# Kernel optimization log

Hardware: AMD Instinct MI355X
Metric: run time of the kernel (lower is better)

## Reference

```python
import jax, jax.numpy as jnp
import numpy as np

DIM = 1024
H = 16
HD = DIM // H          # head_dim = 64
SCALE = HD ** -0.5
LAMBDA_INIT = 0.1


def setup_inputs() -> dict:
    key = jax.random.key(0)
    ks = jax.random.split(key, 8)
    B, NQ, NKV = 4, 1024, 1024
    # xavier_uniform for linear weights; stored as (in, out) for x @ W
    def xavier(k, fan_in, fan_out):
        a = float(np.sqrt(6.0 / (fan_in + fan_out)))
        return jax.random.uniform(k, (fan_in, fan_out), jnp.float32, -a, a)
    return {
        "DriftData": jax.random.normal(ks[0], (B, NQ, DIM), jnp.float32),
        "OceanData": jax.random.normal(ks[1], (B, NKV, DIM), jnp.float32),
        "Wq": xavier(ks[2], DIM, 2 * DIM),
        "Wk": xavier(ks[3], DIM, 2 * DIM),
        "Wv": xavier(ks[4], DIM, DIM),
        "Wo": xavier(ks[5], DIM, DIM),
        "lambda_q1": jax.random.normal(ks[6], (H, HD), jnp.float32),
        "lambda_k1": jax.random.normal(jax.random.fold_in(ks[6], 1), (H, HD), jnp.float32),
        "lambda_q2": jax.random.normal(ks[7], (H, HD), jnp.float32),
        "lambda_k2": jax.random.normal(jax.random.fold_in(ks[7], 1), (H, HD), jnp.float32),
    }


def reference(DriftData, OceanData, Wq, Wk, Wv, Wo,
              lambda_q1, lambda_k1, lambda_q2, lambda_k2):
    B, NQ, dim = DriftData.shape
    NKV = OceanData.shape[1]
    # lambda scalar per head: exp(q1.k1) - exp(q2.k2) + lambda_init  -> (H,)
    lam = (jnp.exp(jnp.sum(lambda_q1 * lambda_k1, axis=-1))
           - jnp.exp(jnp.sum(lambda_q2 * lambda_k2, axis=-1)) + LAMBDA_INIT)
    # projections: Q,K -> 2*dim, V -> dim
    Q = (DriftData @ Wq).reshape(B, NQ, H, 2 * HD).transpose(0, 2, 1, 3)   # b h q 2hd
    K = (OceanData @ Wk).reshape(B, NKV, H, 2 * HD).transpose(0, 2, 1, 3)  # b h k 2hd
    V = (OceanData @ Wv).reshape(B, NKV, H, HD).transpose(0, 2, 1, 3)      # b h k hd
    Q1, Q2 = Q[..., :HD], Q[..., HD:]
    K1, K2 = K[..., :HD], K[..., HD:]
    A1 = jnp.einsum('bhqd,bhkd->bhqk', Q1, K1) * SCALE
    A2 = jnp.einsum('bhqd,bhkd->bhqk', Q2, K2) * SCALE
    att = jax.nn.softmax(A1, axis=-1) - lam[None, :, None, None] * jax.nn.softmax(A2, axis=-1)
    out = jnp.einsum('bhqk,bhkd->bhqd', att, V)            # b h q hd
    out = out.transpose(0, 2, 1, 3).reshape(B, NQ, dim)    # b q dim
    return out @ Wo
```

## Files before the change

kernel.cpp:

```cpp
#include <hip/hip_runtime.h>
#include <hip/hip_bf16.h>

typedef unsigned short u16;
typedef unsigned int u32;
typedef __attribute__((ext_vector_type(8))) short short8;
typedef __attribute__((ext_vector_type(4))) float f32x4;
typedef __attribute__((ext_vector_type(4))) u16 us4;

#define MFMA16(a,b,c) __builtin_amdgcn_mfma_f32_16x16x32_bf16(a,b,c,0,0,0)

__device__ __forceinline__ u16 f2b(float x){
  u32 u = __builtin_bit_cast(u32, x);
  u32 r = (u + 0x7fffu + ((u >> 16) & 1u)) >> 16;
  return (u16)r;
}
__device__ __forceinline__ u16 f2b_hw(float x){
  return __builtin_bit_cast(u16, __float2bfloat16(x));
}

__device__ __forceinline__ void gll16(const u16* g, u16* l){
  __builtin_amdgcn_global_load_lds((const __attribute__((address_space(1))) u32*)g,
                                   (__attribute__((address_space(3))) u32*)l, 16, 0, 0);
}

__global__ __launch_bounds__(256) void k_conv2(const float* __restrict__ a, const float* __restrict__ bsrc,
                                               u16* __restrict__ ya, u16* __restrict__ yb){
  int bid = blockIdx.x;
  const float* x = (bid < 4096) ? a : bsrc;
  u16* y = (bid < 4096) ? ya : yb;
  int i = (bid & 4095) * 256 + threadIdx.x;
  float4 v = reinterpret_cast<const float4*>(x)[i];
  us4 o; o.x = f2b(v.x); o.y = f2b(v.y); o.z = f2b(v.z); o.w = f2b(v.w);
  reinterpret_cast<us4*>(y)[i] = o;
}

__global__ __launch_bounds__(256) void k_prep_w(const float* __restrict__ Wq, const float* __restrict__ Wk,
                                                const float* __restrict__ Wv, const float* __restrict__ Wo,
                                                u16* __restrict__ WqT, u16* __restrict__ WkvT,
                                                u16* __restrict__ WoT,
                                                const float* __restrict__ lq1, const float* __restrict__ lk1,
                                                const float* __restrict__ lq2, const float* __restrict__ lk2,
                                                float* __restrict__ lam){
  __shared__ float t[32][33];
  const int z = blockIdx.z;
  const float* W; u16* WT; int N; float scale = 1.0f;
  if (z == 0){ W = Wq; WT = WqT; N = 2048; scale = 0.125f; }
  else if (z == 1){ W = Wk; WT = WkvT; N = 2048; }
  else if (z == 2){ W = Wv; WT = WkvT + 2048*1024; N = 1024; }
  else { W = Wo; WT = WoT; N = 1024; }
  int n0 = blockIdx.x * 32, k0 = blockIdx.y * 32;
  int tx = threadIdx.x & 31, ty = threadIdx.x >> 5;
  if (n0 < N){
    #pragma unroll
    for (int i = 0; i < 4; i++)
      t[ty + i*8][tx] = W[(size_t)(k0 + ty + i*8) * N + n0 + tx];
    __syncthreads();
    #pragma unroll
    for (int i = 0; i < 4; i++)
      WT[(size_t)(n0 + ty + i*8) * 1024 + k0 + tx] = f2b(t[tx][ty + i*8] * scale);
  }
  if (z == 3 && blockIdx.x == 0 && blockIdx.y == 0 && threadIdx.x < 16){
    int h = threadIdx.x;
    float d1 = 0.f, d2 = 0.f;
    for (int i = 0; i < 64; i++){
      d1 += lq1[h*64 + i] * lk1[h*64 + i];
      d2 += lq2[h*64 + i] * lk2[h*64 + i];
    }
    lam[h] = expf(d1) - expf(d2) + 0.1f;
  }
}

__global__ __launch_bounds__(256) void k_transpose_v(const u16* __restrict__ KV, u16* __restrict__ VT){
  __shared__ u16 t[32][34];
  int kv0 = blockIdx.x * 32, d0 = blockIdx.y * 32, bh = blockIdx.z;
  int b = bh >> 4, h = bh & 15;
  int tx = threadIdx.x & 31, ty = threadIdx.x >> 5;
  #pragma unroll
  for (int i = 0; i < 4; i++)
    t[ty + i*8][tx] = KV[(size_t)(b*1024 + kv0 + ty + i*8) * 3072 + 2048 + h*64 + d0 + tx];
  __syncthreads();
  #pragma unroll
  for (int i = 0; i < 4; i++)
    VT[(size_t)bh * 65536 + (size_t)(d0 + ty + i*8) * 1024 + kv0 + tx] = t[tx][ty + i*8];
}

template<bool OUTF32>
__device__ __forceinline__ void gemm_body(const u16* __restrict__ A, const u16* __restrict__ B,
                                          void* __restrict__ C, int N, int m0, int n0,
                                          u16* As, u16* Bs){
  const int tid = threadIdx.x;
  const int wave = tid >> 6, lane = tid & 63;
  const int lr = lane & 15, lg = lane >> 4;
  const int wm = wave >> 1, wn = wave & 1;

  f32x4 acc[4][4];
  #pragma unroll
  for (int i = 0; i < 4; i++)
    #pragma unroll
    for (int j = 0; j < 4; j++){ f32x4 z = {0.f,0.f,0.f,0.f}; acc[i][j] = z; }

  const int srow = tid >> 3;
  const int skc  = tid & 7;

  for (int k0 = 0; k0 < 1024; k0 += 64){
    #pragma unroll
    for (int c = 0; c < 4; c++){
      int row = c*32 + srow;
      const u16* ga = A + (size_t)(m0 + row) * 1024 + k0 + ((skc ^ (row & 7)) << 3);
      gll16(ga, As + c*2048 + wave*512);
      const u16* gb = B + (size_t)(n0 + row) * 1024 + k0 + ((skc ^ (row & 7)) << 3);
      gll16(gb, Bs + c*2048 + wave*512);
    }
    __syncthreads();
    #pragma unroll
    for (int kc = 0; kc < 2; kc++){
      short8 af[4], bfr[4];
      #pragma unroll
      for (int mt = 0; mt < 4; mt++){
        int row = wm*64 + mt*16 + lr;
        af[mt] = *reinterpret_cast<const short8*>(As + row*64 + (((kc*4 + lg) ^ (row & 7)) << 3));
      }
      #pragma unroll
      for (int nt = 0; nt < 4; nt++){
        int rown = wn*64 + nt*16 + lr;
        bfr[nt] = *reinterpret_cast<const short8*>(Bs + rown*64 + (((kc*4 + lg) ^ (rown & 7)) << 3));
      }
      #pragma unroll
      for (int mt = 0; mt < 4; mt++)
        #pragma unroll
        for (int nt = 0; nt < 4; nt++)
          acc[mt][nt] = MFMA16(af[mt], bfr[nt], acc[mt][nt]);
    }
    __syncthreads();
  }
  #pragma unroll
  for (int mt = 0; mt < 4; mt++)
    #pragma unroll
    for (int nt = 0; nt < 4; nt++)
      #pragma unroll
      for (int r = 0; r < 4; r++){
        int row = m0 + wm*64 + mt*16 + lg*4 + r;
        int col = n0 + wn*64 + nt*16 + lr;
        if (OUTF32) ((float*)C)[(size_t)row * N + col] = acc[mt][nt][r];
        else        ((u16*)C)[(size_t)row * N + col] = f2b(acc[mt][nt][r]);
      }
}

__global__ __launch_bounds__(256) void k_gemm_proj(const u16* __restrict__ Xd, const u16* __restrict__ Xo,
                                                   const u16* __restrict__ WqT, const u16* __restrict__ WkvT,
                                                   u16* __restrict__ Qb, u16* __restrict__ KVb){
  __shared__ __align__(16) u16 As[128*64];
  __shared__ __align__(16) u16 Bs[128*64];
  int bid = blockIdx.x;
  if (bid < 512){
    gemm_body<false>(Xd, WqT, Qb, 2048, (bid >> 4) * 128, (bid & 15) * 128, As, Bs);
  } else {
    int t = bid - 512;
    gemm_body<false>(Xo, WkvT, KVb, 3072, (t / 24) * 128, (t % 24) * 128, As, Bs);
  }
}

__global__ __launch_bounds__(256) void k_gemm_out(const u16* __restrict__ A, const u16* __restrict__ B,
                                                  float* __restrict__ C){
  __shared__ __align__(16) u16 As[128*64];
  __shared__ __align__(16) u16 Bs[128*64];
  int bid = blockIdx.x;
  gemm_body<true>(A, B, C, 1024, (bid >> 3) * 128, (bid & 7) * 128, As, Bs);
}

__device__ __forceinline__ void softmax_t(f32x4 s[4], float& m, float& l, f32x4 (&ob)[4][2], int qt,
                                          u16* pl, int lr, int lg){
  float a0 = fmaxf(fmaxf(s[0][0], s[0][1]), fmaxf(s[0][2], s[0][3]));
  float a1 = fmaxf(fmaxf(s[1][0], s[1][1]), fmaxf(s[1][2], s[1][3]));
  float a2 = fmaxf(fmaxf(s[2][0], s[2][1]), fmaxf(s[2][2], s[2][3]));
  float a3 = fmaxf(fmaxf(s[3][0], s[3][1]), fmaxf(s[3][2], s[3][3]));
  float mx = fmaxf(fmaxf(a0, a1), fmaxf(a2, a3));
  mx = fmaxf(mx, __shfl_xor(mx, 16));
  mx = fmaxf(mx, __shfl_xor(mx, 32));
  if (__any(mx > m + 8.0f)){
    float nm = fmaxf(m, mx);
    float al = __expf(m - nm);
    m = nm; l *= al;
    #pragma unroll
    for (int nt = 0; nt < 4; nt++)
      #pragma unroll
      for (int r = 0; r < 4; r++) ob[nt][qt][r] *= al;
  }
  float sum = 0.f;
  #pragma unroll
  for (int nt = 0; nt < 4; nt++)
    #pragma unroll
    for (int r = 0; r < 4; r++){
      float p = __expf(s[nt][r] - m);
      s[nt][r] = p;
      sum += p;
    }
  sum += __shfl_xor(sum, 16);
  sum += __shfl_xor(sum, 32);
  l += sum;
  char* base = (char*)pl + lr * 128;
  const int swz = (lr & 7) << 4;
  #pragma unroll
  for (int nt = 0; nt < 4; nt++){
    us4 h;
    h.x = f2b_hw(s[nt][0]); h.y = f2b_hw(s[nt][1]);
    h.z = f2b_hw(s[nt][2]); h.w = f2b_hw(s[nt][3]);
    *reinterpret_cast<us4*>(base + ((nt*32 + lg*8) ^ swz)) = h;
  }
}

__global__ __launch_bounds__(256, 2) void k_attn(const u16* __restrict__ Q, const u16* __restrict__ KVb,
                                                 const u16* __restrict__ VT, const float* __restrict__ lam,
                                                 u16* __restrict__ O){
  int bid = blockIdx.x;
  int logical = (bid & 7) * 64 + (bid >> 3);
  int qt8 = logical & 7, h = (logical >> 3) & 15, b = logical >> 7;
  const int tid = threadIdx.x, wave = tid >> 6, lane = tid & 63;
  const int lr = lane & 15, lg = lane >> 4;
  const int qb = qt8 * 128 + wave * 32;

  __shared__ __align__(16) u16 Ks[2][8192];
  __shared__ __align__(16) u16 Vs[2][4096];
  __shared__ __align__(16) u16 Pl[4][2][2][1024];

  const int srow = tid >> 4, schunk = tid & 15;
  const int vrow = tid >> 3, vchunk = tid & 7;
  const u16* Kg = KVb + (size_t)(b*1024 + srow) * 3072 + h*128 + ((schunk ^ (srow & 7)) << 3);
  const u16* Vg = VT + (size_t)(b*16 + h) * 65536 + (size_t)vrow * 1024 + ((vchunk ^ (vrow & 7)) << 3);

  short8 qf[2][2][2];
  #pragma unroll
  for (int qt = 0; qt < 2; qt++){
    const u16* Qp = Q + (size_t)(b*1024 + qb + qt*16 + lr) * 2048 + h*128 + lg*8;
    #pragma unroll
    for (int kc = 0; kc < 2; kc++){
      qf[0][qt][kc] = *reinterpret_cast<const short8*>(Qp + kc*32);
      qf[1][qt][kc] = *reinterpret_cast<const short8*>(Qp + 64 + kc*32);
    }
  }
  const float lamh = lam[h];

  f32x4 o[2][4][2];
  #pragma unroll
  for (int br = 0; br < 2; br++)
    #pragma unroll
    for (int nt = 0; nt < 4; nt++)
      #pragma unroll
      for (int qt = 0; qt < 2; qt++){ f32x4 z = {0.f,0.f,0.f,0.f}; o[br][nt][qt] = z; }
  float m[2][2], l[2][2];
  #pragma unroll
  for (int br = 0; br < 2; br++)
    #pragma unroll
    for (int qt = 0; qt < 2; qt++){ m[br][qt] = -3.0e38f; l[br][qt] = 0.f; }

  auto STAGE = [&](int buf, int kv0){
    u16* kd = &Ks[buf][tid * 8];
    #pragma unroll
    for (int i = 0; i < 4; i++)
      gll16(Kg + (size_t)(kv0 + i*16) * 3072, kd + i*2048);
    u16* vd = &Vs[buf][tid * 8];
    #pragma unroll
    for (int j = 0; j < 2; j++)
      gll16(Vg + kv0 + (size_t)(j*32) * 1024, vd + j*2048);
  };

  STAGE(0, 0);
  __syncthreads();

  for (int t = 0; t < 16; t++){
    const int cur = t & 1;
    if (t < 15) STAGE(cur ^ 1, (t + 1) << 6);

    const u16* kbuf = &Ks[cur][0];
    const u16* vbuf = &Vs[cur][0];

    #pragma unroll
    for (int br = 0; br < 2; br++){
      short8 kf[4][2];
      #pragma unroll
      for (int nt = 0; nt < 4; nt++)
        #pragma unroll
        for (int kc = 0; kc < 2; kc++)
          kf[nt][kc] = *reinterpret_cast<const short8*>(
              kbuf + (nt*16 + lr)*128 + (((br*8 + kc*4 + lg) ^ (lr & 7)) << 3));
      #pragma unroll
      for (int qt = 0; qt < 2; qt++){
        f32x4 s[4];
        #pragma unroll
        for (int nt = 0; nt < 4; nt++){ f32x4 z = {0.f,0.f,0.f,0.f}; s[nt] = z; }
        #pragma unroll
        for (int nt = 0; nt < 4; nt++)
          #pragma unroll
          for (int kc = 0; kc < 2; kc++)
            s[nt] = MFMA16(kf[nt][kc], qf[br][qt][kc], s[nt]);
        softmax_t(s, m[br][qt], l[br][qt], o[br], qt, &Pl[wave][qt][br][0], lr, lg);
      }
    }

    const int swz = (lr & 7) << 4;
    #pragma unroll
    for (int kc = 0; kc < 2; kc++){
      short8 pf[2][2];
      #pragma unroll
      for (int qt = 0; qt < 2; qt++)
        #pragma unroll
        for (int br = 0; br < 2; br++)
          pf[qt][br] = *reinterpret_cast<const short8*>(
              (char*)&Pl[wave][qt][br][0] + lr*128 + ((kc*64 + lg*16) ^ swz));
      #pragma unroll
      for (int nt = 0; nt < 4; nt++){
        short8 vf = *reinterpret_cast<const short8*>(
            vbuf + (nt*16 + lr)*64 + (((kc*4 + lg) ^ (lr & 7)) << 3));
        #pragma unroll
        for (int qt = 0; qt < 2; qt++){
          o[0][nt][qt] = MFMA16(vf, pf[qt][0], o[0][nt][qt]);
          o[1][nt][qt] = MFMA16(vf, pf[qt][1], o[1][nt][qt]);
        }
      }
    }
    __syncthreads();
  }

  #pragma unroll
  for (int qt = 0; qt < 2; qt++){
    const float inv1 = 1.0f / l[0][qt];
    const float inv2 = lamh / l[1][qt];
    u16* Op = O + (size_t)(b*1024 + qb + qt*16 + lr) * 1024 + h*64;
    #pragma unroll
    for (int nt = 0; nt < 4; nt++){
      us4 hh;
      #pragma unroll
      for (int r = 0; r < 4; r++){
        float v = o[0][nt][qt][r] * inv1 - o[1][nt][qt][r] * inv2;
        ((u16*)&hh)[r] = f2b_hw(v);
      }
      *reinterpret_cast<us4*>(Op + nt*16 + lg*4) = hh;
    }
  }
}

extern "C" void kernel_launch(void* const* d_in, const int* in_sizes, int n_in,
                              void* d_out, int out_size, void* d_ws, size_t ws_size,
                              hipStream_t stream){
  const float* Drift = (const float*)d_in[0];
  const float* Ocean = (const float*)d_in[1];
  const float* Wq    = (const float*)d_in[2];
  const float* Wk    = (const float*)d_in[3];
  const float* Wv    = (const float*)d_in[4];
  const float* Wo    = (const float*)d_in[5];
  const float* lq1   = (const float*)d_in[6];
  const float* lk1   = (const float*)d_in[7];
  const float* lq2   = (const float*)d_in[8];
  const float* lk2   = (const float*)d_in[9];
  float* out = (float*)d_out;

  char* ws = (char*)d_ws;
  u16* Xd   = (u16*)(ws);
  u16* Xo   = (u16*)(ws + 8388608);
  u16* WqT  = (u16*)(ws + 16777216);
  u16* WkvT = (u16*)(ws + 20971520);
  u16* WoT  = (u16*)(ws + 27262976);
  u16* Qb   = (u16*)(ws + 29360128);
  u16* KVb  = (u16*)(ws + 46137344);
  u16* VTb  = (u16*)(ws + 71303168);
  u16* Ob   = (u16*)(ws + 79691776);
  float* lam = (float*)(ws + 88080384);

  k_conv2<<<8192, 256, 0, stream>>>(Drift, Ocean, Xd, Xo);
  k_prep_w<<<dim3(64,32,4), 256, 0, stream>>>(Wq, Wk, Wv, Wo, WqT, WkvT, WoT,
                                              lq1, lk1, lq2, lk2, lam);
  k_gemm_proj<<<1280, 256, 0, stream>>>(Xd, Xo, WqT, WkvT, Qb, KVb);
  k_transpose_v<<<dim3(32,2,64), 256, 0, stream>>>(KVb, VTb);
  k_attn<<<512, 256, 0, stream>>>(Qb, KVb, VTb, lam, Ob);
  k_gemm_out<<<256, 256, 0, stream>>>(Ob, WoT, out);
}
```

Before: 155.3 us.

## Fuse V transpose into projection GEMM epilogue, use exp2 softmax and MFMA priority

The V-column tiles of the KV projection GEMM now write their output directly in transposed head-major layout through an LDS staging epilogue. This removes the separate transpose kernel and its extra global round trip. The Q scale now folds in log2(e), so the softmax uses the hardware exp2 directly, and the rescale threshold is adjusted to match. s_setprio raises wave priority around the MFMA sections of attention. The costs are a more complex epilogue with extra barriers, and the KVb V-region is no longer written (attention reads VT only).

Result: slower. 163.0 us (+4.9%).

```diff
diff --git a/kernel.cpp b/kernel.cpp
--- a/kernel.cpp
+++ b/kernel.cpp
@@ -6,6 +6,7 @@
 typedef __attribute__((ext_vector_type(8))) short short8;
 typedef __attribute__((ext_vector_type(4))) float f32x4;
 typedef __attribute__((ext_vector_type(4))) u16 us4;
+typedef __attribute__((ext_vector_type(4))) u32 u32x4;
 
 #define MFMA16(a,b,c) __builtin_amdgcn_mfma_f32_16x16x32_bf16(a,b,c,0,0,0)
 
@@ -17,6 +18,7 @@
 __device__ __forceinline__ u16 f2b_hw(float x){
   return __builtin_bit_cast(u16, __float2bfloat16(x));
 }
+__device__ __forceinline__ float ex2(float x){ return __builtin_amdgcn_exp2f(x); }
 
 __device__ __forceinline__ void gll16(const u16* g, u16* l){
   __builtin_amdgcn_global_load_lds((const __attribute__((address_space(1))) u32*)g,
@@ -44,7 +46,7 @@
   __shared__ float t[32][33];
   const int z = blockIdx.z;
   const float* W; u16* WT; int N; float scale = 1.0f;
-  if (z == 0){ W = Wq; WT = WqT; N = 2048; scale = 0.125f; }
+  if (z == 0){ W = Wq; WT = WqT; N = 2048; scale = 0.1803368867f; }
   else if (z == 1){ W = Wk; WT = WkvT; N = 2048; }
   else if (z == 2){ W = Wv; WT = WkvT + 2048*1024; N = 1024; }
   else { W = Wo; WT = WoT; N = 1024; }
@@ -70,19 +72,45 @@
   }
 }
 
-__global__ __launch_bounds__(256) void k_transpose_v(const u16* __restrict__ KV, u16* __restrict__ VT){
-  __shared__ u16 t[32][34];
-  int kv0 = blockIdx.x * 32, d0 = blockIdx.y * 32, bh = blockIdx.z;
-  int b = bh >> 4, h = bh & 15;
-  int tx = threadIdx.x & 31, ty = threadIdx.x >> 5;
-  #pragma unroll
-  for (int i = 0; i < 4; i++)
-    t[ty + i*8][tx] = KV[(size_t)(b*1024 + kv0 + ty + i*8) * 3072 + 2048 + h*64 + d0 + tx];
-  __syncthreads();
-  #pragma unroll
-  for (int i = 0; i < 4; i++)
-    VT[(size_t)bh * 65536 + (size_t)(d0 + ty + i*8) * 1024 + kv0 + tx] = t[tx][ty + i*8];
-}
+#define GEMM_MAIN_LOOP(A_, B_, m0_, n0_)                                                \
+  f32x4 acc[4][4];                                                                      \
+  _Pragma("unroll")                                                                     \
+  for (int i = 0; i < 4; i++)                                                           \
+    _Pragma("unroll")                                                                   \
+    for (int j = 0; j < 4; j++){ f32x4 z = {0.f,0.f,0.f,0.f}; acc[i][j] = z; }          \
+  const int srow = tid >> 3;                                                            \
+  const int skc  = tid & 7;                                                             \
+  for (int k0 = 0; k0 < 1024; k0 += 64){                                                \
+    _Pragma("unroll")                                                                   \
+    for (int c = 0; c < 4; c++){                                                        \
+      int row = c*32 + srow;                                                            \
+      const u16* ga = (A_) + (size_t)((m0_) + row) * 1024 + k0 + ((skc ^ (row & 7)) << 3); \
+      gll16(ga, As + c*2048 + wave*512);                                                \
+      const u16* gb = (B_) + (size_t)((n0_) + row) * 1024 + k0 + ((skc ^ (row & 7)) << 3); \
+      gll16(gb, Bs + c*2048 + wave*512);                                                \
+    }                                                                                   \
+    __syncthreads();                                                                    \
+    _Pragma("unroll")                                                                   \
+    for (int kc = 0; kc < 2; kc++){                                                     \
+      short8 af[4], bfr[4];                                                             \
+      _Pragma("unroll")                                                                 \
+      for (int mt = 0; mt < 4; mt++){                                                   \
+        int row = wm*64 + mt*16 + lr;                                                   \
+        af[mt] = *reinterpret_cast<const short8*>(As + row*64 + (((kc*4 + lg) ^ (row & 7)) << 3)); \
+      }                                                                                 \
+      _Pragma("unroll")                                                                 \
+      for (int nt = 0; nt < 4; nt++){                                                   \
+        int rown = wn*64 + nt*16 + lr;                                                  \
+        bfr[nt] = *reinterpret_cast<const short8*>(Bs + rown*64 + (((kc*4 + lg) ^ (rown & 7)) << 3)); \
+      }                                                                                 \
+      _Pragma("unroll")                                                                 \
+      for (int mt = 0; mt < 4; mt++)                                                    \
+        _Pragma("unroll")                                                               \
+        for (int nt = 0; nt < 4; nt++)                                                  \
+          acc[mt][nt] = MFMA16(af[mt], bfr[nt], acc[mt][nt]);                           \
+    }                                                                                   \
+    __syncthreads();                                                                    \
+  }
 
 template<bool OUTF32>
 __device__ __forceinline__ void gemm_body(const u16* __restrict__ A, const u16* __restrict__ B,
@@ -92,47 +120,7 @@
   const int wave = tid >> 6, lane = tid & 63;
   const int lr = lane & 15, lg = lane >> 4;
   const int wm = wave >> 1, wn = wave & 1;
-
-  f32x4 acc[4][4];
-  #pragma unroll
-  for (int i = 0; i < 4; i++)
-    #pragma unroll
-    for (int j = 0; j < 4; j++){ f32x4 z = {0.f,0.f,0.f,0.f}; acc[i][j] = z; }
-
-  const int srow = tid >> 3;
-  const int skc  = tid & 7;
-
-  for (int k0 = 0; k0 < 1024; k0 += 64){
-    #pragma unroll
-    for (int c = 0; c < 4; c++){
-      int row = c*32 + srow;
-      const u16* ga = A + (size_t)(m0 + row) * 1024 + k0 + ((skc ^ (row & 7)) << 3);
-      gll16(ga, As + c*2048 + wave*512);
-      const u16* gb = B + (size_t)(n0 + row) * 1024 + k0 + ((skc ^ (row & 7)) << 3);
-      gll16(gb, Bs + c*2048 + wave*512);
-    }
-    __syncthreads();
-    #pragma unroll
-    for (int kc = 0; kc < 2; kc++){
-      short8 af[4], bfr[4];
-      #pragma unroll
-      for (int mt = 0; mt < 4; mt++){
-        int row = wm*64 + mt*16 + lr;
-        af[mt] = *reinterpret_cast<const short8*>(As + row*64 + (((kc*4 + lg) ^ (row & 7)) << 3));
-      }
-      #pragma unroll
-      for (int nt = 0; nt < 4; nt++){
-        int rown = wn*64 + nt*16 + lr;
-        bfr[nt] = *reinterpret_cast<const short8*>(Bs + rown*64 + (((kc*4 + lg) ^ (rown & 7)) << 3));
-      }
-      #pragma unroll
-      for (int mt = 0; mt < 4; mt++)
-        #pragma unroll
-        for (int nt = 0; nt < 4; nt++)
-          acc[mt][nt] = MFMA16(af[mt], bfr[nt], acc[mt][nt]);
-    }
-    __syncthreads();
-  }
+  GEMM_MAIN_LOOP(A, B, m0, n0)
   #pragma unroll
   for (int mt = 0; mt < 4; mt++)
     #pragma unroll
@@ -146,9 +134,53 @@
       }
 }
 
+__device__ __forceinline__ void gemm_body_vt(const u16* __restrict__ A, const u16* __restrict__ B,
+                                             u16* __restrict__ VT, int m0, int n0,
+                                             u16* As, u16* Bs){
+  const int tid = threadIdx.x;
+  const int wave = tid >> 6, lane = tid & 63;
+  const int lr = lane & 15, lg = lane >> 4;
+  const int wm = wave >> 1, wn = wave & 1;
+  GEMM_MAIN_LOOP(A, B, m0, n0)
+  const int vcol0 = n0 - 2048;
+  const int b = m0 >> 10;
+  const int kvbase = m0 & 1023;
+  #pragma unroll
+  for (int c = 0; c < 4; c++){
+    __syncthreads();
+    if (wm == (c >> 1)){
+      #pragma unroll
+      for (int mi = 0; mi < 2; mi++){
+        int mt = (c & 1)*2 + mi;
+        int rl = mi*16 + lg*4;
+        #pragma unroll
+        for (int nt = 0; nt < 4; nt++){
+          int cl = wn*64 + nt*16 + lr;
+          u32 lo = (u32)f2b(acc[mt][nt][0]) | ((u32)f2b(acc[mt][nt][1]) << 16);
+          u32 hi = (u32)f2b(acc[mt][nt][2]) | ((u32)f2b(acc[mt][nt][3]) << 16);
+          u32* p = (u32*)(As + cl*34 + rl);
+          p[0] = lo; p[1] = hi;
+        }
+      }
+    }
+    __syncthreads();
+    int cl = tid >> 1, half = tid & 1;
+    const u32* src = (const u32*)(As + cl*34) + half*8;
+    u32x4 w0, w1;
+    w0.x = src[0]; w0.y = src[1]; w0.z = src[2]; w0.w = src[3];
+    w1.x = src[4]; w1.y = src[5]; w1.z = src[6]; w1.w = src[7];
+    int vcol = vcol0 + cl;
+    int hh = vcol >> 6, dl = vcol & 63;
+    u16* dst = VT + (size_t)(b*16 + hh)*65536 + (size_t)dl*1024 + kvbase + c*32 + half*16;
+    *reinterpret_cast<u32x4*>(dst) = w0;
+    *reinterpret_cast<u32x4*>(dst + 8) = w1;
+  }
+}
+
 __global__ __launch_bounds__(256) void k_gemm_proj(const u16* __restrict__ Xd, const u16* __restrict__ Xo,
                                                    const u16* __restrict__ WqT, const u16* __restrict__ WkvT,
-                                                   u16* __restrict__ Qb, u16* __restrict__ KVb){
+                                                   u16* __restrict__ Qb, u16* __restrict__ KVb,
+                                                   u16* __restrict__ VT){
   __shared__ __align__(16) u16 As[128*64];
   __shared__ __align__(16) u16 Bs[128*64];
   int bid = blockIdx.x;
@@ -156,7 +188,11 @@
     gemm_body<false>(Xd, WqT, Qb, 2048, (bid >> 4) * 128, (bid & 15) * 128, As, Bs);
   } else {
     int t = bid - 512;
-    gemm_body<false>(Xo, WkvT, KVb, 3072, (t / 24) * 128, (t % 24) * 128, As, Bs);
+    int mt8 = t / 24, nt8 = t % 24;
+    if (nt8 < 16)
+      gemm_body<false>(Xo, WkvT, KVb, 3072, mt8 * 128, nt8 * 128, As, Bs);
+    else
+      gemm_body_vt(Xo, WkvT, VT, mt8 * 128, nt8 * 128, As, Bs);
   }
 }
 
@@ -177,9 +213,9 @@
   float mx = fmaxf(fmaxf(a0, a1), fmaxf(a2, a3));
   mx = fmaxf(mx, __shfl_xor(mx, 16));
   mx = fmaxf(mx, __shfl_xor(mx, 32));
-  if (__any(mx > m + 8.0f)){
+  if (__any(mx > m + 11.54f)){
     float nm = fmaxf(m, mx);
-    float al = __expf(m - nm);
+    float al = ex2(m - nm);
     m = nm; l *= al;
     #pragma unroll
     for (int nt = 0; nt < 4; nt++)
@@ -191,7 +227,7 @@
   for (int nt = 0; nt < 4; nt++)
     #pragma unroll
     for (int r = 0; r < 4; r++){
-      float p = __expf(s[nt][r] - m);
+      float p = ex2(s[nt][r] - m);
       s[nt][r] = p;
       sum += p;
     }
@@ -288,16 +324,19 @@
         f32x4 s[4];
         #pragma unroll
         for (int nt = 0; nt < 4; nt++){ f32x4 z = {0.f,0.f,0.f,0.f}; s[nt] = z; }
+        __builtin_amdgcn_s_setprio(1);
         #pragma unroll
         for (int nt = 0; nt < 4; nt++)
           #pragma unroll
           for (int kc = 0; kc < 2; kc++)
             s[nt] = MFMA16(kf[nt][kc], qf[br][qt][kc], s[nt]);
+        __builtin_amdgcn_s_setprio(0);
         softmax_t(s, m[br][qt], l[br][qt], o[br], qt, &Pl[wave][qt][br][0], lr, lg);
       }
     }
 
     const int swz = (lr & 7) << 4;
+    __builtin_amdgcn_s_setprio(1);
     #pragma unroll
     for (int kc = 0; kc < 2; kc++){
       short8 pf[2][2];
@@ -318,6 +357,7 @@
         }
       }
     }
+    __builtin_amdgcn_s_setprio(0);
     __syncthreads();
   }
 
@@ -369,8 +409,7 @@
   k_conv2<<<8192, 256, 0, stream>>>(Drift, Ocean, Xd, Xo);
   k_prep_w<<<dim3(64,32,4), 256, 0, stream>>>(Wq, Wk, Wv, Wo, WqT, WkvT, WoT,
                                               lq1, lk1, lq2, lk2, lam);
-  k_gemm_proj<<<1280, 256, 0, stream>>>(Xd, Xo, WqT, WkvT, Qb, KVb);
-  k_transpose_v<<<dim3(32,2,64), 256, 0, stream>>>(KVb, VTb);
+  k_gemm_proj<<<1280, 256, 0, stream>>>(Xd, Xo, WqT, WkvT, Qb, KVb, VTb);
   k_attn<<<512, 256, 0, stream>>>(Qb, KVb, VTb, lam, Ob);
   k_gemm_out<<<256, 256, 0, stream>>>(Ob, WoT, out);
 }
```

## Split differential attention branches into separate blocks and fuse lambda combine into output GEMM

Applied to the files above, without the earlier changes.

The attention kernel now runs each softmax branch in its own block (1024 blocks, occupancy hint 4), which halves per-block registers and LDS. Each branch writes its normalized output to a separate buffer, reusing the Xd/Xo workspace. The output GEMM loads both buffers, computes O1 - lambda*O2 per head while staging A, and stores it to LDS. Softmax switches to exp2 with log2e folded into the Q weight scale, and s_setprio is placed around the MFMA sections. The cost is that V is loaded twice and the GEMM reads twice as much A data, which it must combine on the fly.

Result: slower. 165.1 us (+6.3%).

```diff
diff --git a/kernel.cpp b/kernel.cpp
--- a/kernel.cpp
+++ b/kernel.cpp
@@ -6,6 +6,7 @@
 typedef __attribute__((ext_vector_type(8))) short short8;
 typedef __attribute__((ext_vector_type(4))) float f32x4;
 typedef __attribute__((ext_vector_type(4))) u16 us4;
+typedef __attribute__((ext_vector_type(4))) u32 u32x4;
 
 #define MFMA16(a,b,c) __builtin_amdgcn_mfma_f32_16x16x32_bf16(a,b,c,0,0,0)
 
@@ -17,6 +18,9 @@
 __device__ __forceinline__ u16 f2b_hw(float x){
   return __builtin_bit_cast(u16, __float2bfloat16(x));
 }
+__device__ __forceinline__ float ex2(float x){ return __builtin_amdgcn_exp2f(x); }
+__device__ __forceinline__ float b2f(u32 lo16){ return __builtin_bit_cast(float, lo16 << 16); }
+__device__ __forceinline__ float b2f_hi(u32 w){ return __builtin_bit_cast(float, w & 0xffff0000u); }
 
 __device__ __forceinline__ void gll16(const u16* g, u16* l){
   __builtin_amdgcn_global_load_lds((const __attribute__((address_space(1))) u32*)g,
@@ -44,7 +48,7 @@
   __shared__ float t[32][33];
   const int z = blockIdx.z;
   const float* W; u16* WT; int N; float scale = 1.0f;
-  if (z == 0){ W = Wq; WT = WqT; N = 2048; scale = 0.125f; }
+  if (z == 0){ W = Wq; WT = WqT; N = 2048; scale = 0.1803368867f; }
   else if (z == 1){ W = Wk; WT = WkvT; N = 2048; }
   else if (z == 2){ W = Wv; WT = WkvT + 2048*1024; N = 1024; }
   else { W = Wo; WT = WoT; N = 1024; }
@@ -160,12 +164,79 @@
   }
 }
 
-__global__ __launch_bounds__(256) void k_gemm_out(const u16* __restrict__ A, const u16* __restrict__ B,
+__global__ __launch_bounds__(256) void k_gemm_out(const u16* __restrict__ O1, const u16* __restrict__ O2,
+                                                  const u16* __restrict__ B, const float* __restrict__ lam,
                                                   float* __restrict__ C){
   __shared__ __align__(16) u16 As[128*64];
   __shared__ __align__(16) u16 Bs[128*64];
   int bid = blockIdx.x;
-  gemm_body<true>(A, B, C, 1024, (bid >> 3) * 128, (bid & 7) * 128, As, Bs);
+  const int m0 = (bid >> 3) * 128, n0 = (bid & 7) * 128;
+  const int tid = threadIdx.x;
+  const int wave = tid >> 6, lane = tid & 63;
+  const int lr = lane & 15, lg = lane >> 4;
+  const int wm = wave >> 1, wn = wave & 1;
+
+  f32x4 acc[4][4];
+  #pragma unroll
+  for (int i = 0; i < 4; i++)
+    #pragma unroll
+    for (int j = 0; j < 4; j++){ f32x4 z = {0.f,0.f,0.f,0.f}; acc[i][j] = z; }
+
+  const int srow = tid >> 3;
+  const int skc  = tid & 7;
+
+  for (int k0 = 0; k0 < 1024; k0 += 64){
+    const float lamh = lam[k0 >> 6];
+    #pragma unroll
+    for (int c = 0; c < 4; c++){
+      int row = c*32 + srow;
+      size_t off = (size_t)(m0 + row) * 1024 + k0 + ((skc ^ (row & 7)) << 3);
+      u32x4 w1 = *reinterpret_cast<const u32x4*>(O1 + off);
+      u32x4 w2 = *reinterpret_cast<const u32x4*>(O2 + off);
+      u32x4 wo;
+      #pragma unroll
+      for (int e = 0; e < 4; e++){
+        u32 a = w1[e], bb = w2[e];
+        float rl = b2f(a & 0xffffu)  - lamh * b2f(bb & 0xffffu);
+        float rh = b2f_hi(a)         - lamh * b2f_hi(bb);
+        wo[e] = (u32)f2b_hw(rl) | ((u32)f2b_hw(rh) << 16);
+      }
+      *reinterpret_cast<u32x4*>(As + c*2048 + tid*8) = wo;
+      const u16* gb = B + (size_t)(n0 + row) * 1024 + k0 + ((skc ^ (row & 7)) << 3);
+      gll16(gb, Bs + c*2048 + wave*512);
+    }
+    __syncthreads();
+    #pragma unroll
+    for (int kc = 0; kc < 2; kc++){
+      short8 af[4], bfr[4];
+      #pragma unroll
+      for (int mt = 0; mt < 4; mt++){
+        int row = wm*64 + mt*16 + lr;
+        af[mt] = *reinterpret_cast<const short8*>(As + row*64 + (((kc*4 + lg) ^ (row & 7)) << 3));
+      }
+      #pragma unroll
+      for (int nt = 0; nt < 4; nt++){
+        int rown = wn*64 + nt*16 + lr;
+        bfr[nt] = *reinterpret_cast<const short8*>(Bs + rown*64 + (((kc*4 + lg) ^ (rown & 7)) << 3));
+      }
+      #pragma unroll
+      for (int mt = 0; mt < 4; mt++)
+        #pragma unroll
+        for (int nt = 0; nt < 4; nt++)
+          acc[mt][nt] = MFMA16(af[mt], bfr[nt], acc[mt][nt]);
+    }
+    __syncthreads();
+  }
+  #pragma unroll
+  for (int mt = 0; mt < 4; mt++)
+    #pragma unroll
+    for (int nt = 0; nt < 4; nt++)
+      #pragma unroll
+      for (int r = 0; r < 4; r++){
+        int row = m0 + wm*64 + mt*16 + lg*4 + r;
+        int col = n0 + wn*64 + nt*16 + lr;
+        C[(size_t)row * 1024 + col] = acc[mt][nt][r];
+      }
 }
 
 __device__ __forceinline__ void softmax_t(f32x4 s[4], float& m, float& l, f32x4 (&ob)[4][2], int qt,
@@ -177,9 +248,9 @@
   float mx = fmaxf(fmaxf(a0, a1), fmaxf(a2, a3));
   mx = fmaxf(mx, __shfl_xor(mx, 16));
   mx = fmaxf(mx, __shfl_xor(mx, 32));
-  if (__any(mx > m + 8.0f)){
+  if (__any(mx > m + 11.54f)){
     float nm = fmaxf(m, mx);
-    float al = __expf(m - nm);
+    float al = ex2(m - nm);
     m = nm; l *= al;
     #pragma unroll
     for (int nt = 0; nt < 4; nt++)
@@ -191,7 +262,7 @@
   for (int nt = 0; nt < 4; nt++)
     #pragma unroll
     for (int r = 0; r < 4; r++){
-      float p = __expf(s[nt][r] - m);
+      float p = ex2(s[nt][r] - m);
       s[nt][r] = p;
       sum += p;
     }
@@ -209,64 +280,51 @@
   }
 }
 
-__global__ __launch_bounds__(256, 2) void k_attn(const u16* __restrict__ Q, const u16* __restrict__ KVb,
-                                                 const u16* __restrict__ VT, const float* __restrict__ lam,
-                                                 u16* __restrict__ O){
+__global__ __launch_bounds__(256, 4) void k_attn(const u16* __restrict__ Q, const u16* __restrict__ KVb,
+                                                 const u16* __restrict__ VT, u16* __restrict__ Obr){
   int bid = blockIdx.x;
-  int logical = (bid & 7) * 64 + (bid >> 3);
-  int qt8 = logical & 7, h = (logical >> 3) & 15, b = logical >> 7;
+  int logical = (bid & 7) * 128 + (bid >> 3);
+  int br = logical & 1, qt8 = (logical >> 1) & 7, h = (logical >> 4) & 15, b = logical >> 8;
   const int tid = threadIdx.x, wave = tid >> 6, lane = tid & 63;
   const int lr = lane & 15, lg = lane >> 4;
   const int qb = qt8 * 128 + wave * 32;
 
-  __shared__ __align__(16) u16 Ks[2][8192];
+  __shared__ __align__(16) u16 Ks[2][4096];
   __shared__ __align__(16) u16 Vs[2][4096];
-  __shared__ __align__(16) u16 Pl[4][2][2][1024];
-
-  const int srow = tid >> 4, schunk = tid & 15;
-  const int vrow = tid >> 3, vchunk = tid & 7;
-  const u16* Kg = KVb + (size_t)(b*1024 + srow) * 3072 + h*128 + ((schunk ^ (srow & 7)) << 3);
-  const u16* Vg = VT + (size_t)(b*16 + h) * 65536 + (size_t)vrow * 1024 + ((vchunk ^ (vrow & 7)) << 3);
-
-  short8 qf[2][2][2];
+  __shared__ __align__(16) u16 Pl[4][1024];
+
+  const int r8 = tid >> 3, ch = tid & 7;
+  const u16* Kg = KVb + (size_t)(b*1024 + r8) * 3072 + h*128 + br*64 + ((ch ^ (r8 & 7)) << 3);
+  const u16* Vg = VT + (size_t)(b*16 + h) * 65536 + (size_t)r8 * 1024 + ((ch ^ (r8 & 7)) << 3);
+
+  short8 qf[2][2];
   #pragma unroll
   for (int qt = 0; qt < 2; qt++){
-    const u16* Qp = Q + (size_t)(b*1024 + qb + qt*16 + lr) * 2048 + h*128 + lg*8;
-    #pragma unroll
-    for (int kc = 0; kc < 2; kc++){
-      qf[0][qt][kc] = *reinterpret_cast<const short8*>(Qp + kc*32);
-      qf[1][qt][kc] = *reinterpret_cast<const short8*>(Qp + 64 + kc*32);
-    }
-  }
-  const float lamh = lam[h];
-
-  f32x4 o[2][4][2];
-  #pragma unroll
-  for (int br = 0; br < 2; br++)
-    #pragma unroll
-    for (int nt = 0; nt < 4; nt++)
-      #pragma unroll
-      for (int qt = 0; qt < 2; qt++){ f32x4 z = {0.f,0.f,0.f,0.f}; o[br][nt][qt] = z; }
-  float m[2][2], l[2][2];
-  #pragma unroll
-  for (int br = 0; br < 2; br++)
-    #pragma unroll
-    for (int qt = 0; qt < 2; qt++){ m[br][qt] = -3.0e38f; l[br][qt] = 0.f; }
+    const u16* Qp = Q + (size_t)(b*1024 + qb + qt*16 + lr) * 2048 + h*128 + br*64 + lg*8;
+    qf[qt][0] = *reinterpret_cast<const short8*>(Qp);
+    qf[qt][1] = *reinterpret_cast<const short8*>(Qp + 32);
+  }
+
+  f32x4 o[4][2];
+  #pragma unroll
+  for (int nt = 0; nt < 4; nt++)
+    #pragma unroll
+    for (int qt = 0; qt < 2; qt++){ f32x4 z = {0.f,0.f,0.f,0.f}; o[nt][qt] = z; }
+  float m[2] = {-3.0e38f, -3.0e38f}, l[2] = {0.f, 0.f};
 
   auto STAGE = [&](int buf, int kv0){
-    u16* kd = &Ks[buf][tid * 8];
-    #pragma unroll
-    for (int i = 0; i < 4; i++)
-      gll16(Kg + (size_t)(kv0 + i*16) * 3072, kd + i*2048);
-    u16* vd = &Vs[buf][tid * 8];
-    #pragma unroll
-    for (int j = 0; j < 2; j++)
-      gll16(Vg + kv0 + (size_t)(j*32) * 1024, vd + j*2048);
+    #pragma unroll
+    for (int i = 0; i < 2; i++)
+      gll16(Kg + (size_t)(kv0 + i*32) * 3072, &Ks[buf][i*2048 + tid*8]);
+    #pragma unroll
+    for (int i = 0; i < 2; i++)
+      gll16(Vg + (size_t)(i*32) * 1024 + kv0, &Vs[buf][i*2048 + tid*8]);
   };
 
   STAGE(0, 0);
   __syncthreads();
 
+  const int swz = (lr & 7) << 4;
   for (int t = 0; t < 16; t++){
     const int cur = t & 1;
     if (t < 15) STAGE(cur ^ 1, (t + 1) << 6);
@@ -275,65 +333,49 @@
     const u16* vbuf = &Vs[cur][0];
 
     #pragma unroll
-    for (int br = 0; br < 2; br++){
-      short8 kf[4][2];
+    for (int qt = 0; qt < 2; qt++){
+      f32x4 s[4];
+      #pragma unroll
+      for (int nt = 0; nt < 4; nt++){ f32x4 z = {0.f,0.f,0.f,0.f}; s[nt] = z; }
+      __builtin_amdgcn_s_setprio(1);
       #pragma unroll
       for (int nt = 0; nt < 4; nt++)
         #pragma unroll
-        for (int kc = 0; kc < 2; kc++)
-          kf[nt][kc] = *reinterpret_cast<const short8*>(
-              kbuf + (nt*16 + lr)*128 + (((br*8 + kc*4 + lg) ^ (lr & 7)) << 3));
-      #pragma unroll
-      for (int qt = 0; qt < 2; qt++){
-        f32x4 s[4];
+        for (int kc = 0; kc < 2; kc++){
+          short8 kfv = *reinterpret_cast<const short8*>(
+              kbuf + (nt*16 + lr)*64 + (((kc*4 + lg) ^ (lr & 7)) << 3));
+          s[nt] = MFMA16(kfv, qf[qt][kc], s[nt]);
+        }
+      __builtin_amdgcn_s_setprio(0);
+      softmax_t(s, m[qt], l[qt], o, qt, &Pl[wave][0], lr, lg);
+      __builtin_amdgcn_s_setprio(1);
+      #pragma unroll
+      for (int kc = 0; kc < 2; kc++){
+        short8 pfv = *reinterpret_cast<const short8*>(
+            (char*)&Pl[wave][0] + lr*128 + ((kc*64 + lg*16) ^ swz));
         #pragma unroll
-        for (int nt = 0; nt < 4; nt++){ f32x4 z = {0.f,0.f,0.f,0.f}; s[nt] = z; }
-        #pragma unroll
-        for (int nt = 0; nt < 4; nt++)
-          #pragma unroll
-          for (int kc = 0; kc < 2; kc++)
-            s[nt] = MFMA16(kf[nt][kc], qf[br][qt][kc], s[nt]);
-        softmax_t(s, m[br][qt], l[br][qt], o[br], qt, &Pl[wave][qt][br][0], lr, lg);
-      }
-    }
-
-    const int swz = (lr & 7) << 4;
-    #pragma unroll
-    for (int kc = 0; kc < 2; kc++){
-      short8 pf[2][2];
-      #pragma unroll
-      for (int qt = 0; qt < 2; qt++)
-        #pragma unroll
-        for (int br = 0; br < 2; br++)
-          pf[qt][br] = *reinterpret_cast<const short8*>(
-              (char*)&Pl[wave][qt][br][0] + lr*128 + ((kc*64 + lg*16) ^ swz));
-      #pragma unroll
-      for (int nt = 0; nt < 4; nt++){
-        short8 vf = *reinterpret_cast<const short8*>(
-            vbuf + (nt*16 + lr)*64 + (((kc*4 + lg) ^ (lr & 7)) << 3));
-        #pragma unroll
-        for (int qt = 0; qt < 2; qt++){
-          o[0][nt][qt] = MFMA16(vf, pf[qt][0], o[0][nt][qt]);
-          o[1][nt][qt] = MFMA16(vf, pf[qt][1], o[1][nt][qt]);
+        for (int nt = 0; nt < 4; nt++){
+          short8 vf = *reinterpret_cast<const short8*>(
+              vbuf + (nt*16 + lr)*64 + (((kc*4 + lg) ^ (lr & 7)) << 3));
+          o[nt][qt] = MFMA16(vf, pfv, o[nt][qt]);
         }
       }
-    }
-    __syncthreads();
-  }
-
+      __builtin_amdgcn_s_setprio(0);
+    }
+    __syncthreads();
+  }
+
+  u16* Ob = Obr + (size_t)br * 4194304;
   #pragma unroll
   for (int qt = 0; qt < 2; qt++){
-    const float inv1 = 1.0f / l[0][qt];
-    const float inv2 = lamh / l[1][qt];
-    u16* Op = O + (size_t)(b*1024 + qb + qt*16 + lr) * 1024 + h*64;
+    const float inv = 1.0f / l[qt];
+    u16* Op = Ob + (size_t)(b*1024 + qb + qt*16 + lr) * 1024 + h*64;
     #pragma unroll
     for (int nt = 0; nt < 4; nt++){
       us4 hh;
       #pragma unroll
-      for (int r = 0; r < 4; r++){
-        float v = o[0][nt][qt][r] * inv1 - o[1][nt][qt][r] * inv2;
-        ((u16*)&hh)[r] = f2b_hw(v);
-      }
+      for (int r = 0; r < 4; r++)
+        ((u16*)&hh)[r] = f2b_hw(o[nt][qt][r] * inv);
       *reinterpret_cast<us4*>(Op + nt*16 + lg*4) = hh;
     }
   }
@@ -357,13 +399,13 @@
   char* ws = (char*)d_ws;
   u16* Xd   = (u16*)(ws);
   u16* Xo   = (u16*)(ws + 8388608);
+  u16* Obr  = (u16*)(ws);
   u16* WqT  = (u16*)(ws + 16777216);
   u16* WkvT = (u16*)(ws + 20971520);
   u16* WoT  = (u16*)(ws + 27262976);
   u16* Qb   = (u16*)(ws + 29360128);
   u16* KVb  = (u16*)(ws + 46137344);
   u16* VTb  = (u16*)(ws + 71303168);
-  u16* Ob   = (u16*)(ws + 79691776);
   float* lam = (float*)(ws + 88080384);
 
   k_conv2<<<8192, 256, 0, stream>>>(Drift, Ocean, Xd, Xo);
@@ -371,6 +413,6 @@
                                               lq1, lk1, lq2, lk2, lam);
   k_gemm_proj<<<1280, 256, 0, stream>>>(Xd, Xo, WqT, WkvT, Qb, KVb);
   k_transpose_v<<<dim3(32,2,64), 256, 0, stream>>>(KVb, VTb);
-  k_attn<<<512, 256, 0, stream>>>(Qb, KVb, VTb, lam, Ob);
-  k_gemm_out<<<256, 256, 0, stream>>>(Ob, WoT, out);
-}
+  k_attn<<<1024, 256, 0, stream>>>(Qb, KVb, VTb, Obr);
+  k_gemm_out<<<256, 256, 0, stream>>>(Obr, Obr + 4194304, WoT, lam, out);
+}
```
